# Performance work log

Measured on AMD Instinct MI355X. Metric: run time of the kernel, lower is better.

## Reference

```python
import jax, jax.numpy as jnp
import numpy as np

R = 128          # input voxel grid resolution
N = 200000
C_IN = 128
C_OUT = 256
G = 32           # group-norm groups
EPS = 1e-5


def _build_sparse_structure():
    """Generate random sparse voxel coords, downsample map, and 3x3x3 neighbor table."""
    rng = np.random.default_rng(0)
    lin = rng.choice(R ** 3, size=N, replace=False)
    cx, cy, cz = lin // (R * R), (lin // R) % R, lin % R
    # downsample by 2: coords // 2 on a (R//2)^3 grid
    Rd = R // 2
    key = ((cx // 2) * Rd + (cy // 2)) * Rd + (cz // 2)
    uk, inv = np.unique(key, return_inverse=True)   # uk sorted
    M = len(uk)
    dx, dy, dz = uk // (Rd * Rd), (uk // Rd) % Rd, uk % Rd
    # 27-neighbor table for submanifold 3x3x3 conv on the downsampled coords
    nbr = np.full((M, 27), -1, np.int32)
    k = 0
    for ox in (-1, 0, 1):
        for oy in (-1, 0, 1):
            for oz in (-1, 0, 1):
                nx, ny, nz = dx + ox, dy + oy, dz + oz
                valid = (nx >= 0) & (nx < Rd) & (ny >= 0) & (ny < Rd) & (nz >= 0) & (nz < Rd)
                nkey = (nx * Rd + ny) * Rd + nz
                pos = np.clip(np.searchsorted(uk, nkey), 0, M - 1)
                found = valid & (uk[pos] == nkey)
                nbr[:, k] = np.where(found, pos, -1).astype(np.int32)
                k += 1
    return inv.astype(np.int32), nbr, M


def setup_inputs() -> dict:
    pool_seg, nbr_idx, M = _build_sparse_structure()
    key = jax.random.key(0)
    ks = jax.random.split(key, 12)
    f32 = jnp.float32
    feats = jax.random.normal(ks[0], (N, C_IN), f32)
    s1 = float(1.0 / np.sqrt(27 * C_IN))
    s2 = float(1.0 / np.sqrt(27 * C_OUT))
    return {
        "feats": feats,
        "gn1_w": 1.0 + 0.1 * jax.random.normal(ks[1], (C_IN,), f32),
        "gn1_b": 0.1 * jax.random.normal(ks[2], (C_IN,), f32),
        "W1": jax.random.normal(ks[3], (27, C_IN, C_OUT), f32) * s1,
        "b1": 0.01 * jax.random.normal(ks[4], (C_OUT,), f32),
        "gn2_w": 1.0 + 0.1 * jax.random.normal(ks[5], (C_OUT,), f32),
        "gn2_b": 0.1 * jax.random.normal(ks[6], (C_OUT,), f32),
        "W2": jax.random.normal(ks[7], (27, C_OUT, C_OUT), f32) * s2,
        "b2": 0.01 * jax.random.normal(ks[8], (C_OUT,), f32),
        "Wskip": jax.random.normal(ks[9], (C_IN, C_OUT), f32) * float(1.0 / np.sqrt(C_IN)),
        "bskip": 0.01 * jax.random.normal(ks[10], (C_OUT,), f32),
        "pool_seg": jnp.asarray(pool_seg),
        "nbr_idx": jnp.asarray(nbr_idx),
        "num_down": int(M),
    }


def _group_norm(x, gamma, beta):
    # batch size 1: normalize each group over all voxels and its channels
    n, c = x.shape
    xg = x.reshape(n, G, c // G)
    mu = xg.mean(axis=(0, 2), keepdims=True)
    var = xg.var(axis=(0, 2), keepdims=True)
    xn = (xg - mu) * jax.lax.rsqrt(var + EPS)
    return xn.reshape(n, c) * gamma + beta


def _sparse_conv3(x, W, b, nbr_idx):
    # submanifold 3x3x3 conv: out[i] = sum_k W[k] @ x[nbr[i,k]] (missing nbr -> 0)
    idx = jnp.maximum(nbr_idx, 0)
    mask = (nbr_idx >= 0).astype(x.dtype)
    acc = jnp.zeros((x.shape[0], W.shape[2]), x.dtype)
    for k in range(27):
        acc = acc + (x[idx[:, k]] * mask[:, k:k + 1]) @ W[k]
    return acc + b


def reference(feats, gn1_w, gn1_b, W1, b1, gn2_w, gn2_b, W2, b2, Wskip, bskip,
              pool_seg, nbr_idx, num_down):
    # act_layers: GroupNorm32 + SiLU on the full-resolution sparse tensor
    h = jax.nn.silu(_group_norm(feats, gn1_w, gn1_b))
    # SparseDownsample(2): average features of voxels sharing a coord//2 cell
    cnt = jax.ops.segment_sum(jnp.ones((feats.shape[0], 1), feats.dtype),
                              pool_seg, num_segments=num_down)
    inv_cnt = 1.0 / jnp.maximum(cnt, 1.0)
    h_d = jax.ops.segment_sum(h, pool_seg, num_segments=num_down) * inv_cnt
    x_d = jax.ops.segment_sum(feats, pool_seg, num_segments=num_down) * inv_cnt
    # out_layers: conv3 -> GN -> SiLU -> conv3
    h1 = _sparse_conv3(h_d, W1, b1, nbr_idx)
    h2 = jax.nn.silu(_group_norm(h1, gn2_w, gn2_b))
    h3 = _sparse_conv3(h2, W2, b2, nbr_idx)
    # skip: 1x1 sparse conv on downsampled input, then add (same coord set)
    skip = x_d @ Wskip + bskip
    return h3 + skip
```

## Files before the change

### kernel.cpp

```cpp
#include <hip/hip_runtime.h>
#include <hip/hip_bf16.h>
#include <stdint.h>

typedef __hip_bfloat16 bf16;
typedef __attribute__((ext_vector_type(8))) __bf16 bf16x8;
typedef __attribute__((ext_vector_type(4))) float f32x4;

#define GN_EPS 1e-5f

__device__ __forceinline__ float silu_f(float x) {
  return x / (1.f + __expf(-x));
}

__device__ __forceinline__ float ldf(const void* p, size_t i, int f) {
  return f ? ((const float*)p)[i]
           : __bfloat162float(((const bf16*)p)[i]);
}

__global__ void detect_k(const void* __restrict__ gn1w, int* __restrict__ flag) {
  if (threadIdx.x == 0 && blockIdx.x == 0) {
    const unsigned short* u = (const unsigned short*)gn1w;
    float mx = 0.f;
    for (int i = 0; i < 128; ++i) {
      unsigned int b = ((unsigned int)u[i]) << 16;
      float v = __uint_as_float(b);
      v = fabsf(v);
      if (!isnan(v) && v > mx) mx = v;
    }
    flag[0] = (mx > 1e4f) ? 1 : 0;
  }
}

__global__ void transpose_k(const void* __restrict__ in, bf16* __restrict__ out,
                            int CI, int CO, const int* __restrict__ flagp) {
  const int f = *flagp;
  int k = blockIdx.y;
  int ntco = CO >> 5;
  int tci = blockIdx.x / ntco, tco = blockIdx.x % ntco;
  __shared__ float t[32][33];
  int tx = threadIdx.x & 31, ty = threadIdx.x >> 5;
  size_t base = (size_t)k * CI * CO;
  bf16* dst = out + base;
#pragma unroll
  for (int j = 0; j < 4; ++j)
    t[ty + 8 * j][tx] =
        ldf(in, base + (size_t)(tci * 32 + ty + 8 * j) * CO + tco * 32 + tx, f);
  __syncthreads();
#pragma unroll
  for (int j = 0; j < 4; ++j)
    dst[(size_t)(tco * 32 + ty + 8 * j) * CI + tci * 32 + tx] =
        __float2bfloat16(t[tx][ty + 8 * j]);
}

__global__ void gn_stats_k(const void* __restrict__ x, float* __restrict__ raw,
                           int rows, int C, const int* __restrict__ flagp) {
  const int f = *flagp;
  int tid = threadIdx.x;
  int rpb = 256 / C;
  int c = tid & (C - 1);
  int stripe = tid / C;
  float s = 0.f, sq = 0.f;
  for (int r = blockIdx.x * rpb + stripe; r < rows; r += gridDim.x * rpb) {
    float v = ldf(x, (size_t)r * C + c, f);
    s += v; sq += v * v;
  }
  __shared__ float ls[256], lq[256];
  ls[tid] = s; lq[tid] = sq;
  __syncthreads();
  if (tid < 32) {
    int per = C >> 5;
    float as = 0.f, aq = 0.f;
    for (int st = 0; st < rpb; ++st)
      for (int e = 0; e < per; ++e) {
        int idx = st * C + tid * per + e;
        as += ls[idx]; aq += lq[idx];
      }
    atomicAdd(&raw[tid], as);
    atomicAdd(&raw[32 + tid], aq);
  }
}

__global__ void gn_fin_k(const float* __restrict__ raw, float* __restrict__ fin,
                         float count) {
  int g = threadIdx.x;
  if (g < 32) {
    float mu = raw[g] / count;
    float var = fmaxf(raw[32 + g] / count - mu * mu, 0.f);
    fin[g] = mu;
    fin[32 + g] = rsqrtf(var + GN_EPS);
  }
}

__global__ void slots_k(const int* __restrict__ seg, int* __restrict__ cnt,
                        int* __restrict__ slots, int N) {
  int i = blockIdx.x * 256 + threadIdx.x;
  if (i >= N) return;
  int s = seg[i];
  int p = atomicAdd(&cnt[s], 1);
  if (p < 8) slots[s * 8 + p] = i;
}

__global__ void down_k(const void* __restrict__ feats, const int* __restrict__ slots,
                       const int* __restrict__ cnt, const float* __restrict__ fin1,
                       const void* __restrict__ gw, const void* __restrict__ gb,
                       bf16* __restrict__ xd, bf16* __restrict__ hd, int M,
                       const int* __restrict__ flagp) {
  const int f = *flagp;
  int cell = blockIdx.x * 2 + (threadIdx.x >> 7);
  int c = threadIdx.x & 127;
  if (cell >= M) return;
  int n = min(cnt[cell], 8);
  int g = c >> 2;
  float mu = fin1[g], is = fin1[32 + g];
  float w = ldf(gw, c, f), b = ldf(gb, c, f);
  float xs = 0.f, hs = 0.f;
  for (int j = 0; j < n; ++j) {
    int v = slots[cell * 8 + j];
    float fv = ldf(feats, (size_t)v * 128 + c, f);
    xs += fv;
    hs += silu_f((fv - mu) * is * w + b);
  }
  float inv = 1.f / (float)max(n, 1);
  xd[(size_t)cell * 128 + c] = __float2bfloat16(xs * inv);
  hd[(size_t)cell * 128 + c] = __float2bfloat16(hs * inv);
}

__global__ void act2_k(bf16* __restrict__ h, const float* __restrict__ fin2,
                       const void* __restrict__ gw, const void* __restrict__ gb,
                       size_t total, const int* __restrict__ flagp) {
  const int f = *flagp;
  size_t i = (size_t)blockIdx.x * 256 + threadIdx.x;
  if (i >= total) return;
  int c = (int)(i & 255);
  int g = c >> 3;
  float v = __bfloat162float(h[i]);
  float t = (v - fin2[g]) * fin2[32 + g] * ldf(gw, c, f) + ldf(gb, c, f);
  h[i] = __float2bfloat16(silu_f(t));
}

template <int CIN, bool SKIP>
__global__ __launch_bounds__(256, 2) void conv_k(
    const bf16* __restrict__ A, const bf16* __restrict__ Wt,
    const void* __restrict__ bias, const void* __restrict__ bias2,
    const bf16* __restrict__ Xd, const int* __restrict__ nbr,
    void* __restrict__ out, int M,
    const int* __restrict__ biasflagp, const int* __restrict__ outflagp) {
  __shared__ alignas(16) char lA[128 * 64];
  __shared__ alignas(16) char lB[128 * 64];
  const int bflag = *biasflagp, oflag = *outflagp;
  const int tid = threadIdx.x;
  const int wave = tid >> 6, lane = tid & 63;
  const int row0 = blockIdx.y * 128, n0 = blockIdx.x * 128;
  const int wr = wave >> 1, wc = wave & 1;
  const int sr = wave * 16 + (lane >> 2);
  const int ch4 = lane & 3;
  const int mrow = lane & 15, quad = lane >> 4;
  const int c1 = n0 + sr;

  f32x4 acc[4][4] = {};

  const int NK = SKIP ? 28 : 27;
  for (int kk = 0; kk < NK; ++kk) {
    const bool isW = (kk < 27);
    const int cink = isW ? CIN : 128;
    const bf16* Ab = isW ? A : Xd;
    const bf16* Wb = Wt + (size_t)(isW ? kk : 27) * (256 * CIN);
    int g1 = row0 + sr, g2 = g1 + 64;
    int src1 = -1, src2 = -1;
    if (isW) {
      if (g1 < M) src1 = nbr[(size_t)g1 * 27 + kk];
      if (g2 < M) src2 = nbr[(size_t)g2 * 27 + kk];
    } else {
      src1 = (g1 < M) ? g1 : -1;
      src2 = (g2 < M) ? g2 : -1;
    }
    const int ncb = cink >> 5;
    for (int cb = 0; cb < ncb; ++cb) {
      uint4 va1 = {0, 0, 0, 0}, va2 = {0, 0, 0, 0};
      if (src1 >= 0)
        va1 = *reinterpret_cast<const uint4*>(Ab + (size_t)src1 * cink + cb * 32 + ch4 * 8);
      if (src2 >= 0)
        va2 = *reinterpret_cast<const uint4*>(Ab + (size_t)src2 * cink + cb * 32 + ch4 * 8);
      uint4 vb1 = *reinterpret_cast<const uint4*>(Wb + (size_t)c1 * cink + cb * 32 + ch4 * 8);
      uint4 vb2 = *reinterpret_cast<const uint4*>(Wb + (size_t)(c1 + 64) * cink + cb * 32 + ch4 * 8);
      *reinterpret_cast<uint4*>(lA + (size_t)sr * 64 + ch4 * 16) = va1;
      *reinterpret_cast<uint4*>(lA + (size_t)(sr + 64) * 64 + ch4 * 16) = va2;
      *reinterpret_cast<uint4*>(lB + (size_t)sr * 64 + ch4 * 16) = vb1;
      *reinterpret_cast<uint4*>(lB + (size_t)(sr + 64) * 64 + ch4 * 16) = vb2;
      __syncthreads();
      bf16x8 af[4], bfr[4];
#pragma unroll
      for (int i = 0; i < 4; ++i)
        af[i] = *reinterpret_cast<const bf16x8*>(
            lA + (size_t)(wr * 64 + i * 16 + mrow) * 64 + quad * 16);
#pragma unroll
      for (int j = 0; j < 4; ++j)
        bfr[j] = *reinterpret_cast<const bf16x8*>(
            lB + (size_t)(wc * 64 + j * 16 + mrow) * 64 + quad * 16);
#pragma unroll
      for (int i = 0; i < 4; ++i)
#pragma unroll
        for (int j = 0; j < 4; ++j)
          acc[i][j] = __builtin_amdgcn_mfma_f32_16x16x32_bf16(af[i], bfr[j],
                                                              acc[i][j], 0, 0, 0);
      __syncthreads();
    }
  }
#pragma unroll
  for (int j = 0; j < 4; ++j) {
    int col = n0 + wc * 64 + j * 16 + mrow;
    float bv = ldf(bias, col, bflag);
    if (SKIP) bv += ldf(bias2, col, bflag);
#pragma unroll
    for (int i = 0; i < 4; ++i) {
      int rb = row0 + wr * 64 + i * 16 + quad * 4;
#pragma unroll
      for (int r = 0; r < 4; ++r) {
        int row = rb + r;
        if (row < M) {
          size_t idx = (size_t)row * 256 + col;
          float val = acc[i][j][r] + bv;
          if (oflag) ((float*)out)[idx] = val;
          else ((bf16*)out)[idx] = __float2bfloat16(val);
        }
      }
    }
  }
}

extern "C" void kernel_launch(void* const* d_in, const int* in_sizes, int n_in,
                              void* d_out, int out_size, void* d_ws, size_t ws_size,
                              hipStream_t stream) {
  const void* feats = d_in[0];
  const void* gn1w = d_in[1];
  const void* gn1b = d_in[2];
  const void* W1 = d_in[3];
  const void* b1 = d_in[4];
  const void* gn2w = d_in[5];
  const void* gn2b = d_in[6];
  const void* W2 = d_in[7];
  const void* b2 = d_in[8];
  const void* Wsk = d_in[9];
  const void* bsk = d_in[10];
  const int* pool = (const int*)d_in[11];
  const int* nbr = (const int*)d_in[12];
  const int N = in_sizes[0] / 128;
  const int M = out_size / 256;

  char* ws = (char*)d_ws;
  auto aup = [](size_t x) { return (x + 255) & ~(size_t)255; };
  float* raw1 = (float*)(ws + 0);
  float* raw2 = (float*)(ws + 256);
  int* flag = (int*)(ws + 512);
  int* zeroflag = (int*)(ws + 516);
  int* cnt = (int*)(ws + 1024);
  size_t o = aup(1024 + (size_t)M * 4);
  float* fin1 = (float*)(ws + o); o += 256;
  float* fin2 = (float*)(ws + o); o += 256;
  int* slots = (int*)(ws + o); o = aup(o + (size_t)M * 32);
  bf16* xd = (bf16*)(ws + o); o += (size_t)M * 256;
  bf16* hd = (bf16*)(ws + o); o += (size_t)M * 256;
  bf16* h1 = (bf16*)(ws + o); o += (size_t)M * 512;
  bf16* wt1 = (bf16*)(ws + o); o += (size_t)27 * 256 * 128 * 2;
  bf16* wt2 = (bf16*)(ws + o); o += ((size_t)27 * 256 * 256 + 256 * 128) * 2;
  (void)ws_size; (void)n_in;

  hipMemsetAsync(ws, 0, 1024 + (size_t)M * 4, stream);

  detect_k<<<1, 64, 0, stream>>>(gn1w, flag);

  transpose_k<<<dim3(4 * 8, 27), 256, 0, stream>>>(W1, wt1, 128, 256, flag);
  transpose_k<<<dim3(8 * 8, 27), 256, 0, stream>>>(W2, wt2, 256, 256, flag);
  transpose_k<<<dim3(4 * 8, 1), 256, 0, stream>>>(
      Wsk, wt2 + (size_t)27 * 256 * 256, 128, 256, flag);

  gn_stats_k<<<512, 256, 0, stream>>>(feats, raw1, N, 128, flag);
  gn_fin_k<<<1, 64, 0, stream>>>(raw1, fin1, (float)N * 4.f);

  slots_k<<<(N + 255) / 256, 256, 0, stream>>>(pool, cnt, slots, N);
  down_k<<<(M + 1) / 2, 256, 0, stream>>>(feats, slots, cnt, fin1, gn1w, gn1b,
                                          xd, hd, M, flag);

  conv_k<128, false><<<dim3(2, (M + 127) / 128), 256, 0, stream>>>(
      hd, wt1, b1, nullptr, nullptr, nbr, h1, M, flag, zeroflag);

  gn_stats_k<<<512, 256, 0, stream>>>(h1, raw2, M, 256, zeroflag);
  gn_fin_k<<<1, 64, 0, stream>>>(raw2, fin2, (float)M * 8.f);
  act2_k<<<(int)(((size_t)M * 256 + 255) / 256), 256, 0, stream>>>(
      h1, fin2, gn2w, gn2b, (size_t)M * 256, flag);

  conv_k<256, true><<<dim3(2, (M + 127) / 128), 256, 0, stream>>>(
      h1, wt2, b2, bsk, xd, nbr, d_out, M, flag, flag);
}
```

Before: 1.550 ms.

## Widen conv tile to all 256 output channels and remap blocks across XCDs

Each conv block now computes all 256 output channels for its 128-row tile instead of half of them. The neighbour gather of A rows happens once per tile rather than twice, so global gather traffic roughly halves. Block indices are also remapped so that consecutive tiles land on the same XCD group (block % 8), which should improve L2 locality for neighbour rows. The cost is double the accumulator registers (128 floats per thread) and larger LDS for B, which may reduce occupancy below the launch-bounds target or cause spills.

```diff
diff --git a/kernel.cpp b/kernel.cpp
--- a/kernel.cpp
+++ b/kernel.cpp
@@ -143,21 +143,23 @@
     const bf16* __restrict__ A, const bf16* __restrict__ Wt,
     const void* __restrict__ bias, const void* __restrict__ bias2,
     const bf16* __restrict__ Xd, const int* __restrict__ nbr,
-    void* __restrict__ out, int M,
+    void* __restrict__ out, int M, int per,
     const int* __restrict__ biasflagp, const int* __restrict__ outflagp) {
   __shared__ alignas(16) char lA[128 * 64];
-  __shared__ alignas(16) char lB[128 * 64];
+  __shared__ alignas(16) char lB[256 * 64];
+  const int nt = (M + 127) >> 7;
+  const int tile = ((int)blockIdx.x % 8) * per + (int)blockIdx.x / 8;
+  if (tile >= nt) return;
   const int bflag = *biasflagp, oflag = *outflagp;
   const int tid = threadIdx.x;
   const int wave = tid >> 6, lane = tid & 63;
-  const int row0 = blockIdx.y * 128, n0 = blockIdx.x * 128;
+  const int row0 = tile * 128;
   const int wr = wave >> 1, wc = wave & 1;
-  const int sr = wave * 16 + (lane >> 2);
-  const int ch4 = lane & 3;
+  const int srow = tid >> 2;
+  const int ch4 = tid & 3;
   const int mrow = lane & 15, quad = lane >> 4;
-  const int c1 = n0 + sr;
-
-  f32x4 acc[4][4] = {};
+
+  f32x4 acc[4][8] = {};
 
   const int NK = SKIP ? 28 : 27;
   for (int kk = 0; kk < NK; ++kk) {
@@ -165,7 +167,7 @@
     const int cink = isW ? CIN : 128;
     const bf16* Ab = isW ? A : Xd;
     const bf16* Wb = Wt + (size_t)(isW ? kk : 27) * (256 * CIN);
-    int g1 = row0 + sr, g2 = g1 + 64;
+    int g1 = row0 + srow, g2 = g1 + 64;
     int src1 = -1, src2 = -1;
     if (isW) {
       if (g1 < M) src1 = nbr[(size_t)g1 * 27 + kk];
@@ -181,34 +183,38 @@
         va1 = *reinterpret_cast<const uint4*>(Ab + (size_t)src1 * cink + cb * 32 + ch4 * 8);
       if (src2 >= 0)
         va2 = *reinterpret_cast<const uint4*>(Ab + (size_t)src2 * cink + cb * 32 + ch4 * 8);
-      uint4 vb1 = *reinterpret_cast<const uint4*>(Wb + (size_t)c1 * cink + cb * 32 + ch4 * 8);
-      uint4 vb2 = *reinterpret_cast<const uint4*>(Wb + (size_t)(c1 + 64) * cink + cb * 32 + ch4 * 8);
-      *reinterpret_cast<uint4*>(lA + (size_t)sr * 64 + ch4 * 16) = va1;
-      *reinterpret_cast<uint4*>(lA + (size_t)(sr + 64) * 64 + ch4 * 16) = va2;
-      *reinterpret_cast<uint4*>(lB + (size_t)sr * 64 + ch4 * 16) = vb1;
-      *reinterpret_cast<uint4*>(lB + (size_t)(sr + 64) * 64 + ch4 * 16) = vb2;
+      uint4 vb[4];
+#pragma unroll
+      for (int r = 0; r < 4; ++r)
+        vb[r] = *reinterpret_cast<const uint4*>(
+            Wb + (size_t)(srow + 64 * r) * cink + cb * 32 + ch4 * 8);
+      *reinterpret_cast<uint4*>(lA + (size_t)srow * 64 + ch4 * 16) = va1;
+      *reinterpret_cast<uint4*>(lA + (size_t)(srow + 64) * 64 + ch4 * 16) = va2;
+#pragma unroll
+      for (int r = 0; r < 4; ++r)
+        *reinterpret_cast<uint4*>(lB + (size_t)(srow + 64 * r) * 64 + ch4 * 16) = vb[r];
       __syncthreads();
-      bf16x8 af[4], bfr[4];
+      bf16x8 af[4], bfr[8];
 #pragma unroll
       for (int i = 0; i < 4; ++i)
         af[i] = *reinterpret_cast<const bf16x8*>(
             lA + (size_t)(wr * 64 + i * 16 + mrow) * 64 + quad * 16);
 #pragma unroll
-      for (int j = 0; j < 4; ++j)
+      for (int j = 0; j < 8; ++j)
         bfr[j] = *reinterpret_cast<const bf16x8*>(
-            lB + (size_t)(wc * 64 + j * 16 + mrow) * 64 + quad * 16);
+            lB + (size_t)(wc * 128 + j * 16 + mrow) * 64 + quad * 16);
 #pragma unroll
       for (int i = 0; i < 4; ++i)
 #pragma unroll
-        for (int j = 0; j < 4; ++j)
+        for (int j = 0; j < 8; ++j)
           acc[i][j] = __builtin_amdgcn_mfma_f32_16x16x32_bf16(af[i], bfr[j],
                                                               acc[i][j], 0, 0, 0);
       __syncthreads();
     }
   }
 #pragma unroll
-  for (int j = 0; j < 4; ++j) {
-    int col = n0 + wc * 64 + j * 16 + mrow;
+  for (int j = 0; j < 8; ++j) {
+    int col = wc * 128 + j * 16 + mrow;
     float bv = ldf(bias, col, bflag);
     if (SKIP) bv += ldf(bias2, col, bflag);
 #pragma unroll
@@ -281,14 +287,18 @@
   down_k<<<(M + 1) / 2, 256, 0, stream>>>(feats, slots, cnt, fin1, gn1w, gn1b,
                                           xd, hd, M, flag);
 
-  conv_k<128, false><<<dim3(2, (M + 127) / 128), 256, 0, stream>>>(
-      hd, wt1, b1, nullptr, nullptr, nbr, h1, M, flag, zeroflag);
+  const int nt = (M + 127) / 128;
+  const int per = (nt + 7) / 8;
+  const int grid = per * 8;
+
+  conv_k<128, false><<<grid, 256, 0, stream>>>(
+      hd, wt1, b1, nullptr, nullptr, nbr, h1, M, per, flag, zeroflag);
 
   gn_stats_k<<<512, 256, 0, stream>>>(h1, raw2, M, 256, zeroflag);
   gn_fin_k<<<1, 64, 0, stream>>>(raw2, fin2, (float)M * 8.f);
   act2_k<<<(int)(((size_t)M * 256 + 255) / 256), 256, 0, stream>>>(
       h1, fin2, gn2w, gn2b, (size_t)M * 256, flag);
 
-  conv_k<256, true><<<dim3(2, (M + 127) / 128), 256, 0, stream>>>(
-      h1, wt2, b2, bsk, xd, nbr, d_out, M, flag, flag);
-}
+  conv_k<256, true><<<grid, 256, 0, stream>>>(
+      h1, wt2, b2, bsk, xd, nbr, d_out, M, per, flag, flag);
+}
```

Result: no change. 1.571 ms (+1.4%).
